# Optimization experiments

Measured on AMD Instinct MI355X. Metric: run time of the kernel, lower is better.

Reference implementation:

```python
import jax, jax.numpy as jnp
import numpy as np


def setup_inputs() -> dict:
    key = jax.random.key(0)
    k1, k2, k3 = jax.random.split(key, 3)
    B, T, H = 64, 512, 1024
    return {
        "encoder_out": jax.random.normal(k1, (B, T, H), dtype=jnp.float32),
        "W_ih": jax.random.normal(k2, (3 * H, H), dtype=jnp.float32) * (1.0 / np.sqrt(H)),
        "W_hh": jax.random.normal(k3, (3 * H, H), dtype=jnp.float32) * (1.0 / np.sqrt(H)),
        "b_ih": jnp.zeros((3 * H,), dtype=jnp.float32),
        "b_hh": jnp.zeros((3 * H,), dtype=jnp.float32),
    }


def reference(encoder_out, W_ih, W_hh, b_ih, b_hh):
    # PyTorch GRUCell semantics; gate order in stacked weights is (r, z, n).
    B, T, H = encoder_out.shape

    # Batch the input-to-hidden projection across all timesteps: [B,T,3H]
    x_proj = jnp.einsum("bth,gh->btg", encoder_out, W_ih) + b_ih
    x_proj_t = jnp.swapaxes(x_proj, 0, 1)  # [T, B, 3H] for scan

    W_hh_T = W_hh.T  # [H, 3H]

    def step(h, xp):
        # recurrent projection: [B, 3H]
        h_proj = h @ W_hh_T + b_hh
        xr, xz, xn = jnp.split(xp, 3, axis=-1)
        hr, hz, hn = jnp.split(h_proj, 3, axis=-1)
        r = jax.nn.sigmoid(xr + hr)
        z = jax.nn.sigmoid(xz + hz)
        n = jnp.tanh(xn + r * hn)
        h_new = (1.0 - z) * n + z * h
        return h_new, h_new

    h0 = jnp.zeros((B, H), dtype=encoder_out.dtype)
    _, h_seq = jax.lax.scan(step, h0, x_proj_t)  # [T, B, H]
    return jnp.swapaxes(h_seq, 0, 1)  # [B, T, H]
```

## Files before the change

kernel.cpp:

```cpp
#include <hip/hip_runtime.h>
#include <hip/hip_bf16.h>


typedef short bf16x8 __attribute__((ext_vector_type(8)));
typedef float f32x4 __attribute__((ext_vector_type(4)));
typedef unsigned int u32x4 __attribute__((ext_vector_type(4)));

#define NB 64
#define NT 512
#define NH 1024
#define NG 3072
#define HWORDS (NB * NH)

static __device__ __forceinline__ float bf2f(unsigned short u) {
    unsigned int x = ((unsigned int)u) << 16;
    float f;
    __builtin_memcpy(&f, &x, sizeof(f));
    return f;
}
static __device__ __forceinline__ unsigned short f2bf(float f) {
    unsigned int x;
    __builtin_memcpy(&x, &f, sizeof(x));
    x += 0x7fffu + ((x >> 16) & 1u);
    return (unsigned short)(x >> 16);
}

static __device__ __forceinline__ f32x4 mfma16(bf16x8 a, bf16x8 b, f32x4 c) {
    return __builtin_amdgcn_mfma_f32_16x16x32_bf16(a, b, c, 0, 0, 0);
}

static __device__ __forceinline__ unsigned umin2(unsigned a, unsigned b) { return a < b ? a : b; }
static __device__ __forceinline__ unsigned umin4(u32x4 a) {
    return umin2(umin2(a[0], a[1]), umin2(a[2], a[3]));
}
static __device__ __forceinline__ bf16x8 pack8(u32x4 a, u32x4 b) {
    union { unsigned u[4]; bf16x8 v; } r;
    r.u[0] = (a[0] & 0xffffu) | (a[1] << 16);
    r.u[1] = (a[2] & 0xffffu) | (a[3] << 16);
    r.u[2] = (b[0] & 0xffffu) | (b[1] << 16);
    r.u[3] = (b[2] & 0xffffu) | (b[3] << 16);
    return r.v;
}

#define GLD16(gp, lp) __builtin_amdgcn_global_load_lds( \
    (const __attribute__((address_space(1))) void*)(gp), \
    (__attribute__((address_space(3))) void*)(lp), 16, 0, 0)

__global__ void k_fill_sentinel(float* __restrict__ o, long n) {
    long i = (long)blockIdx.x * blockDim.x + threadIdx.x;
    if (i < n) o[i] = 12345.0f;
}

__global__ void k_convert(const float* __restrict__ in, unsigned short* __restrict__ o, int n) {
    int i = blockIdx.x * blockDim.x + threadIdx.x;
    if (i < n) o[i] = f2bf(in[i]);
}

__global__ void k_convert_enc(const float* __restrict__ enc, unsigned short* __restrict__ o) {
    long i = (long)blockIdx.x * blockDim.x + threadIdx.x;
    if (i >= (long)NB * NT * NH) return;
    int h = (int)(i % NH);
    long bt = i / NH;
    int t = (int)(bt % NT);
    int b = (int)(bt / NT);
    o[((long)t * NB + b) * NH + h] = f2bf(enc[i]);
}

__global__ void k_init_ht(unsigned int* __restrict__ ht) {
    int i = blockIdx.x * blockDim.x + threadIdx.x;
    ht[i] = 0u;
}

__global__ __launch_bounds__(256) void k_xproj(
    const unsigned short* __restrict__ X,
    const unsigned short* __restrict__ W,
    const float* __restrict__ bias,
    unsigned short* __restrict__ xp)
{
    __shared__ unsigned short As[128 * 32];
    __shared__ unsigned short Bs[128 * 32];

    const int tid  = threadIdx.x;
    const int lane = tid & 63;
    const int wv   = tid >> 6;
    const int l16  = lane & 15;
    const int lq   = lane >> 4;
    const int wr   = wv >> 1;
    const int wc   = wv & 1;
    const int n0   = blockIdx.x * 128;
    const int m0   = blockIdx.y * 128;

    f32x4 acc[4][4];
#pragma unroll
    for (int mi = 0; mi < 4; ++mi)
#pragma unroll
        for (int nj = 0; nj < 4; ++nj) acc[mi][nj] = (f32x4){0.f, 0.f, 0.f, 0.f};

    const int r0 = tid >> 2;
    const int c0e = (tid & 3) * 8;
    const int r1 = (256 + tid) >> 2;

    for (int k0 = 0; k0 < NH; k0 += 32) {
        GLD16(X + (size_t)(m0 + r0) * NH + k0 + c0e, &As[tid * 8]);
        GLD16(X + (size_t)(m0 + r1) * NH + k0 + c0e, &As[(256 + tid) * 8]);
        GLD16(W + (size_t)(n0 + r0) * NH + k0 + c0e, &Bs[tid * 8]);
        GLD16(W + (size_t)(n0 + r1) * NH + k0 + c0e, &Bs[(256 + tid) * 8]);
        __syncthreads();

        bf16x8 a[4], b[4];
#pragma unroll
        for (int mi = 0; mi < 4; ++mi)
            a[mi] = *(const bf16x8*)&As[(wr * 64 + mi * 16 + l16) * 32 + lq * 8];
#pragma unroll
        for (int nj = 0; nj < 4; ++nj)
            b[nj] = *(const bf16x8*)&Bs[(wc * 64 + nj * 16 + l16) * 32 + lq * 8];
#pragma unroll
        for (int mi = 0; mi < 4; ++mi)
#pragma unroll
            for (int nj = 0; nj < 4; ++nj)
                acc[mi][nj] = mfma16(a[mi], b[nj], acc[mi][nj]);
        __syncthreads();
    }

#pragma unroll
    for (int nj = 0; nj < 4; ++nj) {
        int n = n0 + wc * 64 + nj * 16 + l16;
        float bv = bias[n];
        int g   = n >> 10;
        int u   = n & 1023;
        int ugb = u >> 5;
        int ui  = u & 31;
#pragma unroll
        for (int mi = 0; mi < 4; ++mi) {
#pragma unroll
            for (int i = 0; i < 4; ++i) {
                int m = m0 + wr * 64 + mi * 16 + lq * 4 + i;
                int t = m >> 6;
                int b = m & 63;
                xp[(((long)t * 32 + ugb) * 64 + b) * 96 + g * 32 + ui] = f2bf(acc[mi][nj][i] + bv);
            }
        }
    }
}

__global__ __launch_bounds__(512, 1) void k_scan(
    const unsigned short* __restrict__ Whh,
    const float* __restrict__ bhh,
    const unsigned short* __restrict__ xp,
    unsigned int* __restrict__ ht,
    float* __restrict__ out)
{
    const int tid  = threadIdx.x;
    const int lane = tid & 63;
    const int wv   = tid >> 6;
    const int l16  = lane & 15;
    const int lq   = lane >> 4;
    const int bid  = blockIdx.x;
    const int mg   = bid >> 5;
    const int ug   = bid & 31;
    const int m0   = mg * 16;
    const int u0   = ug * 32;
    const int kc0  = wv * 128;

    bf16x8 Bf[3][2][4];
#pragma unroll
    for (int g = 0; g < 3; ++g)
#pragma unroll
        for (int f = 0; f < 2; ++f)
#pragma unroll
            for (int ks = 0; ks < 4; ++ks)
                Bf[g][f][ks] = *(const bf16x8*)(Whh + (long)(g * NH + u0 + f * 16 + l16) * NH + kc0 + ks * 32 + lq * 8);
#pragma unroll
    for (int g = 0; g < 3; ++g)
#pragma unroll
        for (int f = 0; f < 2; ++f)
#pragma unroll
            for (int ks = 0; ks < 4; ++ks)
                asm volatile("" : "+v"(Bf[g][f][ks]));

    const int u_loc = tid & 31;
    const int b_loc = tid >> 5;
    const int b_own = m0 + b_loc;
    const int u_own = u0 + u_loc;
    float bh[3];
#pragma unroll
    for (int g = 0; g < 3; ++g) bh[g] = bhh[g * NH + u_own];
    float hf = 0.0f;

    const int lane_t = (b_loc >> 2) * 16 + (u_loc & 15);
    const int i_t    = b_loc & 3;
    const int shalf  = (u_loc >> 4) * 3;

    __shared__ f32x4 red[8][6][64];

    for (int t = 0; t < NT; ++t) {
        const int slot_r = (t + 3) & 3;
        const int slot_w = t & 3;

        const unsigned short* xpp = xp + (((long)t * 32 + ug) * 64 + b_own) * 96;
        float xr = bf2f(xpp[u_loc]);
        float xz = bf2f(xpp[32 + u_loc]);
        float xn = bf2f(xpp[64 + u_loc]);

        const unsigned int* hp = ht + ((unsigned)(slot_r * NB + m0 + l16) * NH + kc0 + lq * 8);
        const unsigned int thr = (unsigned int)t << 16;
        u32x4 w0, w1, w2, w3, w4, w5, w6, w7;
        for (;;) {
            asm volatile(
                "global_load_dwordx4 %0, %8, off sc0 sc1\n\t"
                "global_load_dwordx4 %1, %8, off offset:16 sc0 sc1\n\t"
                "global_load_dwordx4 %2, %8, off offset:128 sc0 sc1\n\t"
                "global_load_dwordx4 %3, %8, off offset:144 sc0 sc1\n\t"
                "global_load_dwordx4 %4, %8, off offset:256 sc0 sc1\n\t"
                "global_load_dwordx4 %5, %8, off offset:272 sc0 sc1\n\t"
                "global_load_dwordx4 %6, %8, off offset:384 sc0 sc1\n\t"
                "global_load_dwordx4 %7, %8, off offset:400 sc0 sc1\n\t"
                "s_waitcnt vmcnt(0)"
                : "=&v"(w0), "=&v"(w1), "=&v"(w2), "=&v"(w3),
                  "=&v"(w4), "=&v"(w5), "=&v"(w6), "=&v"(w7)
                : "v"(hp) : "memory");
            unsigned m = umin2(umin2(umin4(w0), umin4(w1)), umin2(umin4(w2), umin4(w3)));
            m = umin2(m, umin2(umin2(umin4(w4), umin4(w5)), umin2(umin4(w6), umin4(w7))));
            if (__all(m >= thr)) break;
            __builtin_amdgcn_s_sleep(1);
        }

        bf16x8 av[4];
        av[0] = pack8(w0, w1); av[1] = pack8(w2, w3);
        av[2] = pack8(w4, w5); av[3] = pack8(w6, w7);

        f32x4 acc[2][3];
#pragma unroll
        for (int f = 0; f < 2; ++f)
#pragma unroll
            for (int g = 0; g < 3; ++g) acc[f][g] = (f32x4){0.f, 0.f, 0.f, 0.f};
#pragma unroll
        for (int ks = 0; ks < 4; ++ks)
#pragma unroll
            for (int f = 0; f < 2; ++f)
#pragma unroll
                for (int g = 0; g < 3; ++g)
                    acc[f][g] = mfma16(av[ks], Bf[g][f][ks], acc[f][g]);

#pragma unroll
        for (int f = 0; f < 2; ++f)
#pragma unroll
            for (int g = 0; g < 3; ++g) red[wv][f * 3 + g][lane] = acc[f][g];
        __syncthreads();

        float pre[3];
#pragma unroll
        for (int g = 0; g < 3; ++g) {
            float s = 0.0f;
#pragma unroll
            for (int w = 0; w < 8; ++w) s += red[w][shalf + g][lane_t][i_t];
            pre[g] = s + bh[g];
        }

        float r = 1.0f / (1.0f + __expf(-(xr + pre[0])));
        float z = 1.0f / (1.0f + __expf(-(xz + pre[1])));
        float narg = xn + r * pre[2];
        float nval = 1.0f - 2.0f / (__expf(2.0f * narg) + 1.0f);
        float hnew = (1.0f - z) * nval + z * hf;
        hf = hnew;

        {
            unsigned int* hw = ht + (unsigned)(slot_w * NB + b_own) * NH + u_own;
            unsigned int tv = ((unsigned int)(t + 1) << 16) | (unsigned int)f2bf(hnew);
            asm volatile("global_store_dword %0, %1, off sc0 sc1"
                         :: "v"(hw), "v"(tv) : "memory");
        }
        out[((long)b_own * NT + t) * NH + u_own] = hnew;

        __syncthreads();
    }
}

extern "C" void kernel_launch(void* const* d_in, const int* in_sizes, int n_in,
                              void* d_out, int out_size, void* d_ws, size_t ws_size,
                              hipStream_t stream) {
    const float* enc = (const float*)d_in[0];
    const float* Wih = (const float*)d_in[1];
    const float* Whh = (const float*)d_in[2];
    const float* bih = (const float*)d_in[3];
    const float* bhh = (const float*)d_in[4];
    float* out = (float*)d_out;

    char* p = (char*)d_ws;
    unsigned short* enc_t = (unsigned short*)p; p += (size_t)NT * NB * NH * 2;
    unsigned short* xp    = (unsigned short*)p; p += (size_t)NT * NB * NG * 2;
    unsigned short* wih_b = (unsigned short*)p; p += (size_t)NG * NH * 2;
    unsigned short* whh_b = (unsigned short*)p; p += (size_t)NG * NH * 2;
    size_t need = (size_t)(p - (char*)d_ws);
    unsigned int* ht = (unsigned int*)enc_t;

    if (ws_size < need) {
        long n = (long)out_size;
        k_fill_sentinel<<<(int)((n + 255) / 256), 256, 0, stream>>>(out, n);
        return;
    }

    {
        int n = NG * NH;
        k_convert<<<(n + 255) / 256, 256, 0, stream>>>(Wih, wih_b, n);
        k_convert<<<(n + 255) / 256, 256, 0, stream>>>(Whh, whh_b, n);
        long ne = (long)NB * NT * NH;
        k_convert_enc<<<(int)((ne + 255) / 256), 256, 0, stream>>>(enc, enc_t);
    }

    {
        dim3 grid(NG / 128, (NT * NB) / 128);
        k_xproj<<<grid, 256, 0, stream>>>(enc_t, wih_b, bih, xp);
    }

    k_init_ht<<<4 * HWORDS / 256, 256, 0, stream>>>(ht);

    k_scan<<<128, 512, 0, stream>>>(whh_b, bhh, xp, ht, out);
}
```

Baseline: 2.523 ms.

## Replace tagged hidden-state polling with per-block flags and packed bf16 ring

The recurrent scan used to poll the hidden-state ring directly, where each word carried a timestep tag in its upper half and a bf16 value in its lower half, so every consumer lane repeatedly reloaded 8 dwordx4 per step. Now the hidden state is stored as plain bf16 shorts. Each block publishes a per-(mg,ug) completion flag after a vmcnt wait and a barrier, and one wave spins on the 32 flags of its row group before the block loads 4 dwordx4 of packed bf16 once. This halves the hidden-state traffic, removes the pack/min work, and shrinks the polling footprint, at the cost of an extra block barrier and a flag round-trip on the critical path of every step.

```diff
diff --git a/kernel.cpp b/kernel.cpp
--- a/kernel.cpp
+++ b/kernel.cpp
@@ -4,13 +4,11 @@
 
 typedef short bf16x8 __attribute__((ext_vector_type(8)));
 typedef float f32x4 __attribute__((ext_vector_type(4)));
-typedef unsigned int u32x4 __attribute__((ext_vector_type(4)));
 
 #define NB 64
 #define NT 512
 #define NH 1024
 #define NG 3072
-#define HWORDS (NB * NH)
 
 static __device__ __forceinline__ float bf2f(unsigned short u) {
     unsigned int x = ((unsigned int)u) << 16;
@@ -27,19 +25,6 @@
 
 static __device__ __forceinline__ f32x4 mfma16(bf16x8 a, bf16x8 b, f32x4 c) {
     return __builtin_amdgcn_mfma_f32_16x16x32_bf16(a, b, c, 0, 0, 0);
-}
-
-static __device__ __forceinline__ unsigned umin2(unsigned a, unsigned b) { return a < b ? a : b; }
-static __device__ __forceinline__ unsigned umin4(u32x4 a) {
-    return umin2(umin2(a[0], a[1]), umin2(a[2], a[3]));
-}
-static __device__ __forceinline__ bf16x8 pack8(u32x4 a, u32x4 b) {
-    union { unsigned u[4]; bf16x8 v; } r;
-    r.u[0] = (a[0] & 0xffffu) | (a[1] << 16);
-    r.u[1] = (a[2] & 0xffffu) | (a[3] << 16);
-    r.u[2] = (b[0] & 0xffffu) | (b[1] << 16);
-    r.u[3] = (b[2] & 0xffffu) | (b[3] << 16);
-    return r.v;
 }
 
 #define GLD16(gp, lp) __builtin_amdgcn_global_load_lds( \
@@ -66,9 +51,10 @@
     o[((long)t * NB + b) * NH + h] = f2bf(enc[i]);
 }
 
-__global__ void k_init_ht(unsigned int* __restrict__ ht) {
+#define SYNC_WORDS (4 * NB * NH / 2 + 128)
+__global__ void k_init_sync(unsigned int* __restrict__ base) {
     int i = blockIdx.x * blockDim.x + threadIdx.x;
-    ht[i] = 0u;
+    if (i < SYNC_WORDS) base[i] = 0u;
 }
 
 __global__ __launch_bounds__(256) void k_xproj(
@@ -147,7 +133,8 @@
     const unsigned short* __restrict__ Whh,
     const float* __restrict__ bhh,
     const unsigned short* __restrict__ xp,
-    unsigned int* __restrict__ ht,
+    unsigned short* __restrict__ hring,
+    unsigned* __restrict__ flags,
     float* __restrict__ out)
 {
     const int tid  = threadIdx.x;
@@ -202,32 +189,29 @@
         float xz = bf2f(xpp[32 + u_loc]);
         float xn = bf2f(xpp[64 + u_loc]);
 
-        const unsigned int* hp = ht + ((unsigned)(slot_r * NB + m0 + l16) * NH + kc0 + lq * 8);
-        const unsigned int thr = (unsigned int)t << 16;
-        u32x4 w0, w1, w2, w3, w4, w5, w6, w7;
-        for (;;) {
-            asm volatile(
-                "global_load_dwordx4 %0, %8, off sc0 sc1\n\t"
-                "global_load_dwordx4 %1, %8, off offset:16 sc0 sc1\n\t"
-                "global_load_dwordx4 %2, %8, off offset:128 sc0 sc1\n\t"
-                "global_load_dwordx4 %3, %8, off offset:144 sc0 sc1\n\t"
-                "global_load_dwordx4 %4, %8, off offset:256 sc0 sc1\n\t"
-                "global_load_dwordx4 %5, %8, off offset:272 sc0 sc1\n\t"
-                "global_load_dwordx4 %6, %8, off offset:384 sc0 sc1\n\t"
-                "global_load_dwordx4 %7, %8, off offset:400 sc0 sc1\n\t"
-                "s_waitcnt vmcnt(0)"
-                : "=&v"(w0), "=&v"(w1), "=&v"(w2), "=&v"(w3),
-                  "=&v"(w4), "=&v"(w5), "=&v"(w6), "=&v"(w7)
-                : "v"(hp) : "memory");
-            unsigned m = umin2(umin2(umin4(w0), umin4(w1)), umin2(umin4(w2), umin4(w3)));
-            m = umin2(m, umin2(umin2(umin4(w4), umin4(w5)), umin2(umin4(w6), umin4(w7))));
-            if (__all(m >= thr)) break;
-            __builtin_amdgcn_s_sleep(1);
-        }
-
+        if (t > 0) {
+            if (wv == 0) {
+                const unsigned* fp = flags + mg * 32 + (lane & 31);
+                for (;;) {
+                    unsigned fv;
+                    asm volatile("global_load_dword %0, %1, off sc0 sc1\n\ts_waitcnt vmcnt(0)"
+                                 : "=v"(fv) : "v"(fp) : "memory");
+                    if (__all(fv >= (unsigned)t)) break;
+                }
+            }
+            __syncthreads();
+        }
+
+        const unsigned short* hp = hring + ((slot_r * NB + m0 + l16) * NH + kc0 + lq * 8);
         bf16x8 av[4];
-        av[0] = pack8(w0, w1); av[1] = pack8(w2, w3);
-        av[2] = pack8(w4, w5); av[3] = pack8(w6, w7);
+        asm volatile(
+            "global_load_dwordx4 %0, %4, off sc0 sc1\n\t"
+            "global_load_dwordx4 %1, %4, off offset:64 sc0 sc1\n\t"
+            "global_load_dwordx4 %2, %4, off offset:128 sc0 sc1\n\t"
+            "global_load_dwordx4 %3, %4, off offset:192 sc0 sc1\n\t"
+            "s_waitcnt vmcnt(0)"
+            : "=&v"(av[0]), "=&v"(av[1]), "=&v"(av[2]), "=&v"(av[3])
+            : "v"(hp) : "memory");
 
         f32x4 acc[2][3];
 #pragma unroll
@@ -265,14 +249,19 @@
         hf = hnew;
 
         {
-            unsigned int* hw = ht + (unsigned)(slot_w * NB + b_own) * NH + u_own;
-            unsigned int tv = ((unsigned int)(t + 1) << 16) | (unsigned int)f2bf(hnew);
+            unsigned short* hw = hring + (slot_w * NB + b_own) * NH + u_own;
+            unsigned hv = (unsigned)f2bf(hnew);
+            asm volatile("global_store_short %0, %1, off sc0 sc1"
+                         :: "v"(hw), "v"(hv) : "memory");
+        }
+        asm volatile("s_waitcnt vmcnt(0)" ::: "memory");
+        __syncthreads();
+        if (tid == 0) {
+            unsigned fv = (unsigned)(t + 1);
             asm volatile("global_store_dword %0, %1, off sc0 sc1"
-                         :: "v"(hw), "v"(tv) : "memory");
+                         :: "v"(flags + mg * 32 + ug), "v"(fv) : "memory");
         }
         out[((long)b_own * NT + t) * NH + u_own] = hnew;
-
-        __syncthreads();
     }
 }
 
@@ -292,7 +281,9 @@
     unsigned short* wih_b = (unsigned short*)p; p += (size_t)NG * NH * 2;
     unsigned short* whh_b = (unsigned short*)p; p += (size_t)NG * NH * 2;
     size_t need = (size_t)(p - (char*)d_ws);
-    unsigned int* ht = (unsigned int*)enc_t;
+
+    unsigned short* hring = enc_t;
+    unsigned* flags = (unsigned*)(hring + (size_t)4 * NB * NH);
 
     if (ws_size < need) {
         long n = (long)out_size;
@@ -313,7 +304,7 @@
         k_xproj<<<grid, 256, 0, stream>>>(enc_t, wih_b, bih, xp);
     }
 
-    k_init_ht<<<4 * HWORDS / 256, 256, 0, stream>>>(ht);
-
-    k_scan<<<128, 512, 0, stream>>>(whh_b, bhh, xp, ht, out);
-}
+    k_init_sync<<<(SYNC_WORDS + 255) / 256, 256, 0, stream>>>((unsigned*)hring);
+
+    k_scan<<<128, 512, 0, stream>>>(whh_b, bhh, xp, hring, flags, out);
+}
```

Measured after the change: 2.307 ms. 1.09x faster.
